# Optimization experiments

Hardware: AMD Instinct MI355X
Metric: run time of the kernel (lower is better)

Reference implementation:

```python
import jax, jax.numpy as jnp
import numpy as np

B, S, H, N = 2, 2048, 1024, 16
D = H // N


def setup_inputs() -> dict:
    key = jax.random.key(0)
    k1, k2, k3 = jax.random.split(key, 3)
    # Xavier-uniform-ish init for projection weights
    lim_in = (6.0 / (H + 3 * H)) ** 0.5
    lim_out = (6.0 / (H + H)) ** 0.5
    return {
        "hidden_states": jax.random.normal(k1, (B, S, H), dtype=jnp.float32),
        "w_in": jax.random.uniform(k2, (3 * H, H), minval=-lim_in, maxval=lim_in, dtype=jnp.float32),
        "b_in": jnp.zeros((3 * H,), dtype=jnp.float32),
        "w_out": jax.random.uniform(k3, (H, H), minval=-lim_out, maxval=lim_out, dtype=jnp.float32),
        "b_out": jnp.zeros((H,), dtype=jnp.float32),
    }


def reference(hidden_states, w_in, b_in, w_out, b_out):
    b, s, h = hidden_states.shape
    qkv = hidden_states @ w_in.T + b_in  # [B,S,3H]
    q, k, v = jnp.split(qkv, 3, axis=-1)
    # [B,S,H] -> [B,N,S,D]
    def to_heads(x):
        return x.reshape(b, s, N, D).transpose(0, 2, 1, 3)
    q, k, v = to_heads(q), to_heads(k), to_heads(v)
    scale = D ** -0.5
    scores = jnp.einsum("bnqd,bnkd->bnqk", q, k) * scale  # [B,N,S,S]
    causal = jnp.triu(jnp.ones((s, s), dtype=bool), k=1)
    scores = jnp.where(causal, -jnp.inf, scores)
    attn = jax.nn.softmax(scores, axis=-1)
    out = jnp.einsum("bnqk,bnkd->bnqd", attn, v)  # [B,N,S,D]
    out = out.transpose(0, 2, 1, 3).reshape(b, s, h)
    return out @ w_out.T + b_out
```

## Files before the change

### kernel.cpp

```cpp
#include <hip/hip_runtime.h>
#include <hip/hip_bf16.h>

#define BB 2
#define SS 2048
#define HH 1024
#define NH 16
#define DD 64
#define H3 3072
#define MM (BB*SS)

typedef unsigned short u16;
typedef unsigned int u32;
typedef __attribute__((ext_vector_type(8))) short bf16x8;
typedef __attribute__((ext_vector_type(4))) float f32x4;

__device__ __forceinline__ u16 f2bf(float f) {
    union { float f; u32 u; } v; v.f = f;
    u32 u = v.u;
    u += 0x7fffu + ((u >> 16) & 1u);
    return (u16)(u >> 16);
}
__device__ __forceinline__ float bf2f(u16 h) {
    union { u32 u; float f; } v; v.u = ((u32)h) << 16;
    return v.f;
}
__device__ __forceinline__ u32 pack2bf(float a, float b) {
    __hip_bfloat162 h = __float22bfloat162_rn(float2{a, b});
    u32 u; __builtin_memcpy(&u, &h, 4);
    return u;
}
__device__ __forceinline__ void gl_lds16(const void* g, void* l) {
    __builtin_amdgcn_global_load_lds(
        (const __attribute__((address_space(1))) u32*)g,
        (__attribute__((address_space(3))) u32*)l, 16, 0, 0);
}

__global__ void cvt3bf(const float4* __restrict__ s0, uint2* __restrict__ d0, int n0,
                       const float4* __restrict__ s1, uint2* __restrict__ d1, int n1,
                       const float4* __restrict__ s2, uint2* __restrict__ d2, int n2) {
    int i = blockIdx.x * blockDim.x + threadIdx.x;
    const int tot = n0 + n1 + n2;
    for (; i < tot; i += gridDim.x * blockDim.x) {
        const float4* s; uint2* d; int j;
        if (i < n0)            { s = s0; d = d0; j = i; }
        else if (i < n0 + n1)  { s = s1; d = d1; j = i - n0; }
        else                   { s = s2; d = d2; j = i - n0 - n1; }
        float4 v = s[j];
        uint2 o; o.x = pack2bf(v.x, v.y); o.y = pack2bf(v.z, v.w);
        d[j] = o;
    }
}

template<int BN, int MODE>
__global__ __launch_bounds__(256, 2)
void gemm_k2(const u16* __restrict__ A, const u16* __restrict__ Bbf,
             const u16* __restrict__ biasbf, void* __restrict__ Cptr,
             u16* __restrict__ Qo, u16* __restrict__ Ko, u16* __restrict__ Vto,
             int M, int Nn, int K)
{
    constexpr int NFR = BN / 32;
    __shared__ __align__(16) u16 Alds[128 * 32];
    __shared__ __align__(16) u16 Blds[BN * 32];
    const int tid = threadIdx.x;
    const int w = tid >> 6, lane = tid & 63, quad = lane >> 4, l16 = lane & 15;
    const int m0 = blockIdx.x * 128, n0 = blockIdx.y * BN;
    const int wm = w >> 1, wn = w & 1;
    const int rA4 = lane >> 2, c8b = (lane & 3) * 8;

    f32x4 acc[4][NFR] = {};

    for (int k0 = 0; k0 < K; k0 += 32) {
        __syncthreads();
#pragma unroll
        for (int q = 0; q < 2; ++q) {
            int row0 = w * 32 + q * 16;
            gl_lds16(&A[(size_t)(m0 + row0 + rA4) * K + k0 + c8b], &Alds[row0 * 32]);
        }
#pragma unroll
        for (int q = 0; q < BN / 64; ++q) {
            int row0 = w * (BN / 4) + q * 16;
            gl_lds16(&Bbf[(size_t)(n0 + row0 + rA4) * K + k0 + c8b], &Blds[row0 * 32]);
        }
        __syncthreads();

        bf16x8 af[4], bfr[NFR];
#pragma unroll
        for (int mi = 0; mi < 4; ++mi)
            af[mi] = *(const bf16x8*)&Alds[(wm * 64 + mi * 16 + l16) * 32 + quad * 8];
#pragma unroll
        for (int ni = 0; ni < NFR; ++ni)
            bfr[ni] = *(const bf16x8*)&Blds[(wn * (BN / 2) + ni * 16 + l16) * 32 + quad * 8];
#pragma unroll
        for (int mi = 0; mi < 4; ++mi)
#pragma unroll
            for (int ni = 0; ni < NFR; ++ni)
                acc[mi][ni] = __builtin_amdgcn_mfma_f32_16x16x32_bf16(
                    af[mi], bfr[ni], acc[mi][ni], 0, 0, 0);
    }

#pragma unroll
    for (int mi = 0; mi < 4; ++mi) {
        int row_b = m0 + wm * 64 + mi * 16 + quad * 4;
#pragma unroll
        for (int ni = 0; ni < NFR; ++ni) {
            int col = n0 + wn * (BN / 2) + ni * 16 + l16;
            float bv = bf2f(biasbf[col]);
            if constexpr (MODE == 1) {
#pragma unroll
                for (int i = 0; i < 4; ++i)
                    ((float*)Cptr)[(size_t)(row_b + i) * Nn + col] = acc[mi][ni][i] + bv;
            } else {
                if (col < 1024) {
#pragma unroll
                    for (int i = 0; i < 4; ++i)
                        Qo[(size_t)(row_b + i) * 1024 + col] =
                            f2bf((acc[mi][ni][i] + bv) * 0.125f);
                } else if (col < 2048) {
#pragma unroll
                    for (int i = 0; i < 4; ++i)
                        Ko[(size_t)(row_b + i) * 1024 + (col - 1024)] =
                            f2bf(acc[mi][ni][i] + bv);
                } else {
                    int d = col - 2048, hh = d >> 6, dd = d & 63;
                    int b = row_b >> 11, s = row_b & 2047;
                    u16 t0 = f2bf(acc[mi][ni][0] + bv), t1 = f2bf(acc[mi][ni][1] + bv);
                    u16 t2 = f2bf(acc[mi][ni][2] + bv), t3 = f2bf(acc[mi][ni][3] + bv);
                    uint2 pk; pk.x = (u32)t0 | ((u32)t1 << 16);
                    pk.y = (u32)t2 | ((u32)t3 << 16);
                    *(uint2*)&Vto[((size_t)((b * 16 + hh) * 64 + dd)) * 2048 + s] = pk;
                }
            }
        }
    }
}

__global__ __launch_bounds__(256, 2)
void attn_v3(const u16* __restrict__ Q, const u16* __restrict__ Kb,
             const u16* __restrict__ Vt, u16* __restrict__ attn_out) {
    const int pr = blockIdx.x, h = blockIdx.y, b = blockIdx.z;
    const int tid = threadIdx.x;
    const int w = tid >> 6, lane = tid & 63, quad = lane >> 4, l16 = lane & 15;
    __shared__ __align__(16) u16 Klds[2][64 * 72];
    __shared__ __align__(16) u16 Vlds[2][64 * 72];
    __shared__ __align__(16) u16 Pb[4][16 * 72];
    const int r0 = tid >> 3, cc8 = (tid & 7) * 8;

    for (int half = 0; half < 2; ++half) {
        const int qt = half ? pr : (31 - pr);
        const int q0 = qt * 64;
        const int T = qt + 1;

        const u16* Qb = Q  + (size_t)(b * SS + q0) * 1024 + h * 64;
        const u16* Kg = Kb + (size_t)(b * SS) * 1024 + h * 64;
        const u16* Vg = Vt + (size_t)((b * 16 + h) * 64) * 2048;

        bf16x8 qf0 = *(const bf16x8*)&Qb[(size_t)(w * 16 + l16) * 1024 + quad * 8];
        bf16x8 qf1 = *(const bf16x8*)&Qb[(size_t)(w * 16 + l16) * 1024 + 32 + quad * 8];

        f32x4 oacc[4] = {};
        float lp[4] = {0.f, 0.f, 0.f, 0.f};

        uint4 kr0 = *(const uint4*)&Kg[(size_t)r0 * 1024 + cc8];
        uint4 kr1 = *(const uint4*)&Kg[(size_t)(r0 + 32) * 1024 + cc8];
        uint4 vr0 = *(const uint4*)&Vg[(size_t)r0 * 2048 + cc8];
        uint4 vr1 = *(const uint4*)&Vg[(size_t)(r0 + 32) * 2048 + cc8];
        __syncthreads();
        *(uint4*)&Klds[0][r0 * 72 + cc8]        = kr0;
        *(uint4*)&Klds[0][(r0 + 32) * 72 + cc8] = kr1;
        *(uint4*)&Vlds[0][r0 * 72 + cc8]        = vr0;
        *(uint4*)&Vlds[0][(r0 + 32) * 72 + cc8] = vr1;

        for (int t = 0; t < T; ++t) {
            const int cur = t & 1;
            __syncthreads();
            if (t + 1 < T) {
                const int nv = (t + 1) * 64;
                kr0 = *(const uint4*)&Kg[(size_t)(nv + r0) * 1024 + cc8];
                kr1 = *(const uint4*)&Kg[(size_t)(nv + r0 + 32) * 1024 + cc8];
                vr0 = *(const uint4*)&Vg[(size_t)r0 * 2048 + nv + cc8];
                vr1 = *(const uint4*)&Vg[(size_t)(r0 + 32) * 2048 + nv + cc8];
            }
            f32x4 sacc[4] = {};
#pragma unroll
            for (int ni = 0; ni < 4; ++ni) {
                bf16x8 kf0 = *(const bf16x8*)&Klds[cur][(ni * 16 + l16) * 72 + quad * 8];
                bf16x8 kf1 = *(const bf16x8*)&Klds[cur][(ni * 16 + l16) * 72 + 32 + quad * 8];
                sacc[ni] = __builtin_amdgcn_mfma_f32_16x16x32_bf16(qf0, kf0, sacc[ni], 0, 0, 0);
                sacc[ni] = __builtin_amdgcn_mfma_f32_16x16x32_bf16(qf1, kf1, sacc[ni], 0, 0, 0);
            }
            const int kv0 = t * 64;
#pragma unroll
            for (int ni = 0; ni < 4; ++ni) {
                int colg = kv0 + ni * 16 + l16;
#pragma unroll
                for (int i = 0; i < 4; ++i) {
                    int rowg = q0 + w * 16 + quad * 4 + i;
                    float p = (colg <= rowg) ? __expf(sacc[ni][i]) : 0.f;
                    lp[i] += p;
                    Pb[w][(quad * 4 + i) * 72 + ni * 16 + l16] = f2bf(p);
                }
            }
            bf16x8 pf0 = *(const bf16x8*)&Pb[w][l16 * 72 + quad * 8];
            bf16x8 pf1 = *(const bf16x8*)&Pb[w][l16 * 72 + 32 + quad * 8];
#pragma unroll
            for (int ni = 0; ni < 4; ++ni) {
                bf16x8 vf0 = *(const bf16x8*)&Vlds[cur][(ni * 16 + l16) * 72 + quad * 8];
                bf16x8 vf1 = *(const bf16x8*)&Vlds[cur][(ni * 16 + l16) * 72 + 32 + quad * 8];
                oacc[ni] = __builtin_amdgcn_mfma_f32_16x16x32_bf16(pf0, vf0, oacc[ni], 0, 0, 0);
                oacc[ni] = __builtin_amdgcn_mfma_f32_16x16x32_bf16(pf1, vf1, oacc[ni], 0, 0, 0);
            }
            if (t + 1 < T) {
                const int nxt = cur ^ 1;
                *(uint4*)&Klds[nxt][r0 * 72 + cc8]        = kr0;
                *(uint4*)&Klds[nxt][(r0 + 32) * 72 + cc8] = kr1;
                *(uint4*)&Vlds[nxt][r0 * 72 + cc8]        = vr0;
                *(uint4*)&Vlds[nxt][(r0 + 32) * 72 + cc8] = vr1;
            }
        }

#pragma unroll
        for (int i = 0; i < 4; ++i) {
#pragma unroll
            for (int s = 1; s < 16; s <<= 1)
                lp[i] += __shfl_xor(lp[i], s, 64);
            lp[i] = 1.0f / lp[i];
        }
        u16* ob = attn_out + (size_t)(b * SS + q0 + w * 16) * 1024 + h * 64;
#pragma unroll
        for (int ni = 0; ni < 4; ++ni)
#pragma unroll
            for (int i = 0; i < 4; ++i)
                ob[(size_t)(quad * 4 + i) * 1024 + ni * 16 + l16] =
                    f2bf(oacc[ni][i] * lp[i]);
    }
}

extern "C" void kernel_launch(void* const* d_in, const int* in_sizes, int n_in,
                              void* d_out, int out_size, void* d_ws, size_t ws_size,
                              hipStream_t stream) {
    const float* hidden = (const float*)d_in[0];
    const float* w_in   = (const float*)d_in[1];
    const float* b_in   = (const float*)d_in[2];
    const float* w_out  = (const float*)d_in[3];
    const float* b_out  = (const float*)d_in[4];
    float* out = (float*)d_out;

    char* ws = (char*)d_ws;
    u16* hid_bf  = (u16*)d_out;
    u16* wi_bf   = (u16*)ws;
    u16* bi_bf   = (u16*)(ws + 6291456);
    u16* attn_ws = (u16*)ws;
    u16* Qbuf    = (u16*)(ws + 8388608);
    u16* wo_bf   = (u16*)(ws + 8388608);
    u16* bo_bf   = (u16*)(ws + 8388608 + 2097152);
    u16* Kbuf    = (u16*)(ws + 16777216);
    u16* Vtbuf   = (u16*)(ws + 25165824);

    cvt3bf<<<dim3(2048), dim3(256), 0, stream>>>(
        (const float4*)hidden, (uint2*)hid_bf, 1048576,
        (const float4*)w_in,   (uint2*)wi_bf,  786432,
        (const float4*)b_in,   (uint2*)bi_bf,  768);
    gemm_k2<128, 2><<<dim3(32, 24), dim3(256), 0, stream>>>(
        hid_bf, wi_bf, bi_bf, nullptr, Qbuf, Kbuf, Vtbuf, MM, H3, HH);
    attn_v3<<<dim3(16, NH, BB), dim3(256), 0, stream>>>(
        Qbuf, Kbuf, Vtbuf, attn_ws);
    cvt3bf<<<dim3(512), dim3(256), 0, stream>>>(
        (const float4*)w_out, (uint2*)wo_bf, 262144,
        (const float4*)b_out, (uint2*)bo_bf, 256,
        nullptr, nullptr, 0);
    gemm_k2<64, 1><<<dim3(32, 16), dim3(256), 0, stream>>>(
        attn_ws, wo_bf, bo_bf, out, nullptr, nullptr, nullptr, MM, HH, HH);
}
```

Measured before the change: 187.0 us.

## Switch attention to 32x32 MFMA tiles with 128-row query blocks

The attention kernel now uses 32x32x16 bf16 MFMA instructions, with each wave owning 32 query rows and each block covering 128 query rows. This replaces the earlier scheme where each block processed two 64-row tiles paired for causal load balance. Larger MFMA tiles raise the compute done per LDS fragment load and halve the K/V tile loads per query row. The cost is uneven per-block work, since blocks now run from 2 to 32 KV tiles with no pairing, and more accumulator registers per thread.

```diff
diff --git a/kernel.cpp b/kernel.cpp
--- a/kernel.cpp
+++ b/kernel.cpp
@@ -13,6 +13,7 @@
 typedef unsigned int u32;
 typedef __attribute__((ext_vector_type(8))) short bf16x8;
 typedef __attribute__((ext_vector_type(4))) float f32x4;
+typedef __attribute__((ext_vector_type(16))) float f32x16;
 
 __device__ __forceinline__ u16 f2bf(float f) {
     union { float f; u32 u; } v; v.f = f;
@@ -135,104 +136,111 @@
 }
 
 __global__ __launch_bounds__(256, 2)
-void attn_v3(const u16* __restrict__ Q, const u16* __restrict__ Kb,
+void attn_v4(const u16* __restrict__ Q, const u16* __restrict__ Kb,
              const u16* __restrict__ Vt, u16* __restrict__ attn_out) {
-    const int pr = blockIdx.x, h = blockIdx.y, b = blockIdx.z;
+    const int qt = 15 - blockIdx.x, h = blockIdx.y, b = blockIdx.z;
     const int tid = threadIdx.x;
-    const int w = tid >> 6, lane = tid & 63, quad = lane >> 4, l16 = lane & 15;
+    const int w = tid >> 6, lane = tid & 63;
+    const int l32 = lane & 31, h5 = lane >> 5;
     __shared__ __align__(16) u16 Klds[2][64 * 72];
     __shared__ __align__(16) u16 Vlds[2][64 * 72];
-    __shared__ __align__(16) u16 Pb[4][16 * 72];
+    __shared__ __align__(16) u16 Pb[4][32 * 72];
     const int r0 = tid >> 3, cc8 = (tid & 7) * 8;
 
-    for (int half = 0; half < 2; ++half) {
-        const int qt = half ? pr : (31 - pr);
-        const int q0 = qt * 64;
-        const int T = qt + 1;
-
-        const u16* Qb = Q  + (size_t)(b * SS + q0) * 1024 + h * 64;
-        const u16* Kg = Kb + (size_t)(b * SS) * 1024 + h * 64;
-        const u16* Vg = Vt + (size_t)((b * 16 + h) * 64) * 2048;
-
-        bf16x8 qf0 = *(const bf16x8*)&Qb[(size_t)(w * 16 + l16) * 1024 + quad * 8];
-        bf16x8 qf1 = *(const bf16x8*)&Qb[(size_t)(w * 16 + l16) * 1024 + 32 + quad * 8];
-
-        f32x4 oacc[4] = {};
-        float lp[4] = {0.f, 0.f, 0.f, 0.f};
-
-        uint4 kr0 = *(const uint4*)&Kg[(size_t)r0 * 1024 + cc8];
-        uint4 kr1 = *(const uint4*)&Kg[(size_t)(r0 + 32) * 1024 + cc8];
-        uint4 vr0 = *(const uint4*)&Vg[(size_t)r0 * 2048 + cc8];
-        uint4 vr1 = *(const uint4*)&Vg[(size_t)(r0 + 32) * 2048 + cc8];
+    const int q0 = qt * 128;
+    const int qw = q0 + w * 32;
+    const int T = 2 * (qt + 1);
+
+    const u16* Qb = Q  + (size_t)(b * SS) * 1024 + h * 64;
+    const u16* Kg = Kb + (size_t)(b * SS) * 1024 + h * 64;
+    const u16* Vg = Vt + (size_t)((b * 16 + h) * 64) * 2048;
+
+    bf16x8 qf[4];
+#pragma unroll
+    for (int kt = 0; kt < 4; ++kt)
+        qf[kt] = *(const bf16x8*)&Qb[(size_t)(qw + l32) * 1024 + kt * 16 + h5 * 8];
+
+    f32x16 oacc[2] = {};
+    float lp[16];
+#pragma unroll
+    for (int j = 0; j < 16; ++j) lp[j] = 0.f;
+
+    uint4 kr0 = *(const uint4*)&Kg[(size_t)r0 * 1024 + cc8];
+    uint4 kr1 = *(const uint4*)&Kg[(size_t)(r0 + 32) * 1024 + cc8];
+    uint4 vr0 = *(const uint4*)&Vg[(size_t)r0 * 2048 + cc8];
+    uint4 vr1 = *(const uint4*)&Vg[(size_t)(r0 + 32) * 2048 + cc8];
+    *(uint4*)&Klds[0][r0 * 72 + cc8]        = kr0;
+    *(uint4*)&Klds[0][(r0 + 32) * 72 + cc8] = kr1;
+    *(uint4*)&Vlds[0][r0 * 72 + cc8]        = vr0;
+    *(uint4*)&Vlds[0][(r0 + 32) * 72 + cc8] = vr1;
+
+    for (int t = 0; t < T; ++t) {
+        const int cur = t & 1;
+        const int kv0 = t * 64;
         __syncthreads();
-        *(uint4*)&Klds[0][r0 * 72 + cc8]        = kr0;
-        *(uint4*)&Klds[0][(r0 + 32) * 72 + cc8] = kr1;
-        *(uint4*)&Vlds[0][r0 * 72 + cc8]        = vr0;
-        *(uint4*)&Vlds[0][(r0 + 32) * 72 + cc8] = vr1;
-
-        for (int t = 0; t < T; ++t) {
-            const int cur = t & 1;
-            __syncthreads();
-            if (t + 1 < T) {
-                const int nv = (t + 1) * 64;
-                kr0 = *(const uint4*)&Kg[(size_t)(nv + r0) * 1024 + cc8];
-                kr1 = *(const uint4*)&Kg[(size_t)(nv + r0 + 32) * 1024 + cc8];
-                vr0 = *(const uint4*)&Vg[(size_t)r0 * 2048 + nv + cc8];
-                vr1 = *(const uint4*)&Vg[(size_t)(r0 + 32) * 2048 + nv + cc8];
-            }
-            f32x4 sacc[4] = {};
-#pragma unroll
-            for (int ni = 0; ni < 4; ++ni) {
-                bf16x8 kf0 = *(const bf16x8*)&Klds[cur][(ni * 16 + l16) * 72 + quad * 8];
-                bf16x8 kf1 = *(const bf16x8*)&Klds[cur][(ni * 16 + l16) * 72 + 32 + quad * 8];
-                sacc[ni] = __builtin_amdgcn_mfma_f32_16x16x32_bf16(qf0, kf0, sacc[ni], 0, 0, 0);
-                sacc[ni] = __builtin_amdgcn_mfma_f32_16x16x32_bf16(qf1, kf1, sacc[ni], 0, 0, 0);
-            }
-            const int kv0 = t * 64;
-#pragma unroll
-            for (int ni = 0; ni < 4; ++ni) {
-                int colg = kv0 + ni * 16 + l16;
-#pragma unroll
-                for (int i = 0; i < 4; ++i) {
-                    int rowg = q0 + w * 16 + quad * 4 + i;
-                    float p = (colg <= rowg) ? __expf(sacc[ni][i]) : 0.f;
-                    lp[i] += p;
-                    Pb[w][(quad * 4 + i) * 72 + ni * 16 + l16] = f2bf(p);
-                }
-            }
-            bf16x8 pf0 = *(const bf16x8*)&Pb[w][l16 * 72 + quad * 8];
-            bf16x8 pf1 = *(const bf16x8*)&Pb[w][l16 * 72 + 32 + quad * 8];
-#pragma unroll
-            for (int ni = 0; ni < 4; ++ni) {
-                bf16x8 vf0 = *(const bf16x8*)&Vlds[cur][(ni * 16 + l16) * 72 + quad * 8];
-                bf16x8 vf1 = *(const bf16x8*)&Vlds[cur][(ni * 16 + l16) * 72 + 32 + quad * 8];
-                oacc[ni] = __builtin_amdgcn_mfma_f32_16x16x32_bf16(pf0, vf0, oacc[ni], 0, 0, 0);
-                oacc[ni] = __builtin_amdgcn_mfma_f32_16x16x32_bf16(pf1, vf1, oacc[ni], 0, 0, 0);
-            }
-            if (t + 1 < T) {
-                const int nxt = cur ^ 1;
-                *(uint4*)&Klds[nxt][r0 * 72 + cc8]        = kr0;
-                *(uint4*)&Klds[nxt][(r0 + 32) * 72 + cc8] = kr1;
-                *(uint4*)&Vlds[nxt][r0 * 72 + cc8]        = vr0;
-                *(uint4*)&Vlds[nxt][(r0 + 32) * 72 + cc8] = vr1;
-            }
-        }
-
-#pragma unroll
-        for (int i = 0; i < 4; ++i) {
-#pragma unroll
-            for (int s = 1; s < 16; s <<= 1)
-                lp[i] += __shfl_xor(lp[i], s, 64);
-            lp[i] = 1.0f / lp[i];
-        }
-        u16* ob = attn_out + (size_t)(b * SS + q0 + w * 16) * 1024 + h * 64;
-#pragma unroll
-        for (int ni = 0; ni < 4; ++ni)
-#pragma unroll
-            for (int i = 0; i < 4; ++i)
-                ob[(size_t)(quad * 4 + i) * 1024 + ni * 16 + l16] =
-                    f2bf(oacc[ni][i] * lp[i]);
-    }
+        if (t + 1 < T) {
+            const int nv = kv0 + 64;
+            kr0 = *(const uint4*)&Kg[(size_t)(nv + r0) * 1024 + cc8];
+            kr1 = *(const uint4*)&Kg[(size_t)(nv + r0 + 32) * 1024 + cc8];
+            vr0 = *(const uint4*)&Vg[(size_t)r0 * 2048 + nv + cc8];
+            vr1 = *(const uint4*)&Vg[(size_t)(r0 + 32) * 2048 + nv + cc8];
+        }
+        f32x16 sacc[2] = {};
+#pragma unroll
+        for (int nt = 0; nt < 2; ++nt)
+#pragma unroll
+            for (int kt = 0; kt < 4; ++kt) {
+                bf16x8 kf = *(const bf16x8*)
+                    &Klds[cur][(nt * 32 + l32) * 72 + kt * 16 + h5 * 8];
+                sacc[nt] = __builtin_amdgcn_mfma_f32_32x32x16_bf16(
+                    qf[kt], kf, sacc[nt], 0, 0, 0);
+            }
+#pragma unroll
+        for (int nt = 0; nt < 2; ++nt) {
+            int colg = kv0 + nt * 32 + l32;
+#pragma unroll
+            for (int j = 0; j < 16; ++j) {
+                int rl = (j & 3) + 8 * (j >> 2) + 4 * h5;
+                float p = (colg <= qw + rl) ? __expf(sacc[nt][j]) : 0.f;
+                lp[j] += p;
+                Pb[w][rl * 72 + nt * 32 + l32] = f2bf(p);
+            }
+        }
+#pragma unroll
+        for (int kt = 0; kt < 4; ++kt) {
+            bf16x8 pa = *(const bf16x8*)&Pb[w][l32 * 72 + kt * 16 + h5 * 8];
+#pragma unroll
+            for (int nt = 0; nt < 2; ++nt) {
+                bf16x8 vf = *(const bf16x8*)
+                    &Vlds[cur][(nt * 32 + l32) * 72 + kt * 16 + h5 * 8];
+                oacc[nt] = __builtin_amdgcn_mfma_f32_32x32x16_bf16(
+                    pa, vf, oacc[nt], 0, 0, 0);
+            }
+        }
+        if (t + 1 < T) {
+            const int nxt = cur ^ 1;
+            *(uint4*)&Klds[nxt][r0 * 72 + cc8]        = kr0;
+            *(uint4*)&Klds[nxt][(r0 + 32) * 72 + cc8] = kr1;
+            *(uint4*)&Vlds[nxt][r0 * 72 + cc8]        = vr0;
+            *(uint4*)&Vlds[nxt][(r0 + 32) * 72 + cc8] = vr1;
+        }
+    }
+
+#pragma unroll
+    for (int j = 0; j < 16; ++j) {
+#pragma unroll
+        for (int s = 1; s < 32; s <<= 1)
+            lp[j] += __shfl_xor(lp[j], s, 64);
+        lp[j] = 1.0f / lp[j];
+    }
+    u16* ob = attn_out + (size_t)(b * SS + qw) * 1024 + h * 64;
+#pragma unroll
+    for (int nt = 0; nt < 2; ++nt)
+#pragma unroll
+        for (int j = 0; j < 16; ++j) {
+            int rl = (j & 3) + 8 * (j >> 2) + 4 * h5;
+            ob[(size_t)rl * 1024 + nt * 32 + l32] = f2bf(oacc[nt][j] * lp[j]);
+        }
 }
 
 extern "C" void kernel_launch(void* const* d_in, const int* in_sizes, int n_in,
@@ -262,7 +270,7 @@
         (const float4*)b_in,   (uint2*)bi_bf,  768);
     gemm_k2<128, 2><<<dim3(32, 24), dim3(256), 0, stream>>>(
         hid_bf, wi_bf, bi_bf, nullptr, Qbuf, Kbuf, Vtbuf, MM, H3, HH);
-    attn_v3<<<dim3(16, NH, BB), dim3(256), 0, stream>>>(
+    attn_v4<<<dim3(16, NH, BB), dim3(256), 0, stream>>>(
         Qbuf, Kbuf, Vtbuf, attn_ws);
     cvt3bf<<<dim3(512), dim3(256), 0, stream>>>(
         (const float4*)w_out, (uint2*)wo_bf, 262144,
```

New measurement: 202.0 us. +8.0%, slower.
